# Performance work log

Measured on AMD Instinct MI355X. Metric: run time of the kernel, lower is better.

Reference implementation:

```python
import jax, jax.numpy as jnp
import numpy as np

LAMBDA = 0.7
RATIO = 3
EPS = 1e-6


def setup_inputs() -> dict:
    key = jax.random.key(0)
    k1, k2, k3 = jax.random.split(key, 3)
    bs, n, w, h = 8, 7, 640, 640
    preds = jax.random.normal(k1, (bs, n, w, h), dtype=jnp.float32)
    labels = jax.random.randint(k2, (bs, n, w, h), 0, 2, dtype=jnp.int32)
    training_mask = jax.random.randint(k3, (bs, w, h), 0, 2, dtype=jnp.int32)
    return {"preds": preds, "labels": labels, "training_mask": training_mask}


def _dice(S, G):
    # S, G: [C, P]; per-channel dice coefficient, then mean over channels
    num = 2.0 * jnp.sum(S * G, axis=-1)
    den = jnp.sum(S * S, axis=-1) + jnp.sum(G * G, axis=-1) + EPS
    return jnp.mean(num / den)


def _single_sample(pred, label, mask):
    # pred, label: [n, P]; mask: [P]
    P = pred.shape[-1]
    p = jax.nn.sigmoid(pred)
    pred_n = p[-1] * mask            # masked full-text prediction
    label_n = label[-1] * mask

    # --- OHEM mask M (cal_M): keep all positives + top (ratio*n_pos) hardest negatives ---
    pos = pred_n >= 0.5
    n_pos = jnp.sum(pos)
    n_neg_all = jnp.sum(~pos)
    k = n_pos * RATIO
    # sigmoid outputs are in (0,1); sentinel -1 pushes positives to the end of the descending sort
    neg_vals = jnp.where(pos, -1.0, pred_n)
    sorted_desc = -jnp.sort(-neg_vals)
    thr = sorted_desc[jnp.clip(k - 1, 0, P - 1)]  # k-th largest negative score
    ohem_active = (n_neg_all > k) & (k > 0)
    M = jnp.where(ohem_active, (pred_n >= thr).astype(jnp.float32), 1.0)

    # L_c: dice loss on OHEM-selected full-text map
    L_c = 1.0 - _dice((pred_n * M)[None, :], (label_n * M)[None, :])

    # L_s: dice loss on shrunk kernels, gated by predicted text region W
    W = (pred_n >= 0.5).astype(jnp.float32)
    L_s = 1.0 - _dice(p[:-1] * W, label[:-1] * W)

    loss = LAMBDA * L_c + (1.0 - LAMBDA) * L_s
    return L_c, L_s, loss


def reference(preds, labels, training_mask):
    bs, n, w, h = preds.shape
    preds = preds.reshape(bs, n, w * h)
    labels = labels.reshape(bs, n, w * h).astype(jnp.float32)
    mask = training_mask.reshape(bs, w * h).astype(jnp.float32)
    L_c, L_s, loss = jax.vmap(_single_sample)(preds, labels, mask)
    # reduction='mean'
    return L_c.mean(), L_s.mean(), loss.mean()
```

## Files before the change

### kernel.cpp

```cpp
#include <hip/hip_runtime.h>

#define BS   8
#define NCH  7
#define PX   409600
#define NBIN 65536
#define NCHK 256
#define EPSF 1e-6f
#define NT   256
#define GXA  200
#define UA   2
#define GXB  50
#define UB   4
#define ITB  2
#define NWAVE 1600

__device__ __forceinline__ float sigf(float x) {
    return 1.0f / (1.0f + __expf(-x));
}

__device__ __forceinline__ unsigned wred_u(unsigned v) {
    #pragma unroll
    for (int o = 32; o; o >>= 1) v += __shfl_down(v, o);
    return v;
}

__device__ __forceinline__ float wred_f(float v) {
    #pragma unroll
    for (int o = 32; o; o >>= 1) v += __shfl_down(v, o);
    return v;
}

__device__ __forceinline__ void wred3_f(float& v0, float& v1, float& v2) {
    #pragma unroll
    for (int o = 32; o; o >>= 1) {
        float t0 = __shfl_down(v0, o);
        float t1 = __shfl_down(v1, o);
        float t2 = __shfl_down(v2, o);
        v0 += t0; v1 += t1; v2 += t2;
    }
}

__device__ void select2(const unsigned* __restrict__ chunks,
                        const unsigned* __restrict__ bins,
                        unsigned k, unsigned* out_bin, unsigned* out_rank) {
    __shared__ unsigned cs[256];
    int t = threadIdx.x;
    cs[t] = chunks[t];
    __syncthreads();
    #pragma unroll
    for (int off = 1; off < 256; off <<= 1) {
        unsigned v = cs[t];
        unsigned a = (t + off < 256) ? cs[t + off] : 0u;
        __syncthreads();
        cs[t] = v + a;
        __syncthreads();
    }
    {
        unsigned sfx  = cs[t];
        unsigned sfx1 = (t < 255) ? cs[t + 1] : 0u;
        if (sfx >= k && sfx1 < k) { *out_bin = (unsigned)t; *out_rank = k - sfx1; }
    }
    __syncthreads();
    unsigned chunk = *out_bin, krem = *out_rank;
    cs[t] = bins[chunk * 256 + t];
    __syncthreads();
    #pragma unroll
    for (int off = 1; off < 256; off <<= 1) {
        unsigned v = cs[t];
        unsigned a = (t + off < 256) ? cs[t + off] : 0u;
        __syncthreads();
        cs[t] = v + a;
        __syncthreads();
    }
    {
        unsigned sfx  = cs[t];
        unsigned sfx1 = (t < 255) ? cs[t + 1] : 0u;
        if (sfx >= krem && sfx1 < krem) {
            *out_bin  = chunk * 256 + (unsigned)t;
            *out_rank = krem - sfx1;
        }
    }
    __syncthreads();
}

__global__ __launch_bounds__(256) void k_a(
        const float* __restrict__ preds, const int* __restrict__ labels,
        const int* __restrict__ mask,
        float* __restrict__ psumA,
        unsigned* __restrict__ ppos,
        unsigned* __restrict__ pzero,
        unsigned long long* __restrict__ wm,
        unsigned* __restrict__ done) {
    const int tid = threadIdx.x;
    const int b = blockIdx.y, cb = blockIdx.x;
    if (b == 0 && cb == 0 && tid == 0) *done = 0u;

    const float* pr6 = preds + ((size_t)b * NCH + 6) * PX;
    const int*   lb6 = labels + ((size_t)b * NCH + 6) * PX;
    const int*   mk  = mask + (size_t)b * PX;
    const int g0 = cb * (NT * UA) + tid;
    const int lane = tid & 63, wid = tid >> 6;

    float4 P[UA]; int4 L[UA]; int4 M[UA];
    #pragma unroll
    for (int q = 0; q < UA; q++) {
        int px = (g0 + q * NT) * 4;
        P[q] = *(const float4*)(pr6 + px);
        L[q] = *(const int4*)(lb6 + px);
        M[q] = *(const int4*)(mk + px);
    }

    float a0 = 0.f, a1 = 0.f;
    unsigned a2c = 0, pos = 0, zer = 0;
    #pragma unroll
    for (int q = 0; q < UA; q++) {
        float mm[4]  = {(float)M[q].x, (float)M[q].y, (float)M[q].z, (float)M[q].w};
        float pa[4]  = {P[q].x, P[q].y, P[q].z, P[q].w};
        int   la[4]  = {L[q].x, L[q].y, L[q].z, L[q].w};
        unsigned long long bp[4];
        #pragma unroll
        for (int v = 0; v < 4; v++) {
            float pn = sigf(pa[v]) * mm[v];
            bp[v] = __ballot(pn >= 0.5f);
            unsigned long long bz = __ballot(__float_as_uint(pn) == 0u);
            pos += (unsigned)__popcll(bp[v]);
            zer += (unsigned)__popcll(bz);
            bool ln = (la[v] != 0) & (M[q].x == M[q].x) & (mm[v] != 0.0f);
            a0 += ln ? pn : 0.0f;
            a1 += pn * pn;
            a2c += ln ? 1u : 0u;
        }
        if (lane == 0) {
            int wv = (g0 + q * NT) >> 6;
            ulonglong2* wp = (ulonglong2*)(wm + ((size_t)b * NWAVE + wv) * 4);
            wp[0] = make_ulonglong2(bp[0], bp[1]);
            wp[1] = make_ulonglong2(bp[2], bp[3]);
        }
    }

    __shared__ unsigned cpos[4], czer[4];
    __shared__ float red[4][3];
    if (lane == 0) { cpos[wid] = pos; czer[wid] = zer; }
    float v0 = a0, v1 = a1, v2 = (float)a2c;
    wred3_f(v0, v1, v2);
    if (lane == 0) { red[wid][0] = v0; red[wid][1] = v1; red[wid][2] = v2; }
    __syncthreads();
    if (tid < 3) {
        float tot = red[0][tid] + red[1][tid] + red[2][tid] + red[3][tid];
        psumA[((size_t)b * 3 + tid) * GXA + cb] = tot;
    }
    if (tid == 3) ppos[b * GXA + cb]  = cpos[0] + cpos[1] + cpos[2] + cpos[3];
    if (tid == 4) pzero[b * GXA + cb] = czer[0] + czer[1] + czer[2] + czer[3];
}

__global__ __launch_bounds__(256) void k_b(
        const float* __restrict__ preds, const int* __restrict__ labels,
        const unsigned long long* __restrict__ wm,
        float* __restrict__ psumB) {
    const int tid = threadIdx.x;
    const int y = blockIdx.y;
    const int b = y / 6, c = y % 6;
    const int cb = blockIdx.x;
    const int lane = tid & 63;
    const int widu = __builtin_amdgcn_readfirstlane(tid >> 6);
    const float* pc = preds + ((size_t)b * NCH + c) * PX;
    const int*   lc = labels + ((size_t)b * NCH + c) * PX;
    const unsigned long long* wmb = wm + (size_t)b * NWAVE * 4;

    float sn = 0.f, sp = 0.f;
    unsigned slc = 0;

    for (int it = 0; it < ITB; ++it) {
        const int gbase = cb * (NT * UB * ITB) + it * (NT * UB) + tid;
        float4 P[UB]; int4 L[UB];
        #pragma unroll
        for (int q = 0; q < UB; q++) {
            int px = (gbase + q * NT) * 4;
            P[q] = *(const float4*)(pc + px);
            L[q] = *(const int4*)(lc + px);
        }
        ulonglong2 WA[UB], WB[UB];
        #pragma unroll
        for (int q = 0; q < UB; q++) {
            int wv = ((cb * (NT * UB * ITB) + it * (NT * UB) + q * NT) >> 6) + widu;
            const ulonglong2* wp = (const ulonglong2*)(wmb + (size_t)wv * 4);
            WA[q] = wp[0];
            WB[q] = wp[1];
        }
        #pragma unroll
        for (int q = 0; q < UB; q++) {
            float pa[4] = {P[q].x, P[q].y, P[q].z, P[q].w};
            int   la[4] = {L[q].x, L[q].y, L[q].z, L[q].w};
            unsigned wbit[4] = {
                (unsigned)((WA[q].x >> lane) & 1ull), (unsigned)((WA[q].y >> lane) & 1ull),
                (unsigned)((WB[q].x >> lane) & 1ull), (unsigned)((WB[q].y >> lane) & 1ull) };
            #pragma unroll
            for (int v = 0; v < 4; v++) {
                float s = sigf(pa[v]);
                bool w  = wbit[v] != 0u;
                bool lw = w && (la[v] != 0);
                sn += lw ? s : 0.0f;
                sp += w ? s * s : 0.0f;
                slc += lw ? 1u : 0u;
            }
        }
    }

    __shared__ float red[4][3];
    float v0 = sn, v1 = sp, v2 = (float)slc;
    wred3_f(v0, v1, v2);
    if (lane == 0) { red[tid >> 6][0] = v0; red[tid >> 6][1] = v1; red[tid >> 6][2] = v2; }
    __syncthreads();
    if (tid < 3) {
        float tot = red[0][tid] + red[1][tid] + red[2][tid] + red[3][tid];
        psumB[((size_t)y * 3 + tid) * GXB + cb] = tot;
    }
}

__global__ __launch_bounds__(256) void k_sel(
        const float* __restrict__ preds, const int* __restrict__ labels,
        const int* __restrict__ mask,
        const float* __restrict__ psumA, const float* __restrict__ psumB,
        const unsigned* __restrict__ ppos, const unsigned* __restrict__ pzero,
        unsigned* __restrict__ histws, unsigned* __restrict__ chunkws,
        float* __restrict__ lcls, unsigned* __restrict__ done,
        float* __restrict__ out) {
    const int tid = threadIdx.x;
    const int b = blockIdx.x;
    const int lane = tid & 63, wid = tid >> 6;

    __shared__ float S[21];
    __shared__ unsigned C[2];
    if (tid < 21) S[tid] = 0.f;
    if (tid < 2) C[tid] = 0u;
    __syncthreads();
    {
        unsigned pc = 0, zc = 0;
        for (int i = tid; i < GXA; i += NT) {
            pc += ppos[b * GXA + i];
            zc += pzero[b * GXA + i];
        }
        pc = wred_u(pc); zc = wred_u(zc);
        if (lane == 0) { atomicAdd(&C[0], pc); atomicAdd(&C[1], zc); }
    }
    for (int i = tid; i < 3 * GXA; i += NT)
        atomicAdd(&S[18 + i / GXA], psumA[(size_t)b * 3 * GXA + i]);
    for (int i = tid; i < 6 * 3 * GXB; i += NT) {
        int cch = i / (3 * GXB);
        int j   = (i / GXB) % 3;
        atomicAdd(&S[j * 6 + cch], psumB[(size_t)b * 6 * 3 * GXB + i]);
    }
    __syncthreads();
    const unsigned np = C[0], zc = C[1];

    const unsigned k = np * 3u;
    const bool active = ((unsigned)PX - np > k) && (k > 0u);
    const unsigned nzneg = (unsigned)PX - np - zc;

    float Lc_b;
    if (!active || k >= nzneg) {
        Lc_b = 1.0f - 2.0f * S[18] / (S[19] + S[20] + EPSF);
    } else {
        unsigned* h1 = histws + (size_t)b * NBIN;
        unsigned* c1 = chunkws + (size_t)b * NCHK;
        const float* pr6 = preds + ((size_t)b * NCH + 6) * PX;
        const int*   lb6 = labels + ((size_t)b * NCH + 6) * PX;
        const int*   mk  = mask + (size_t)b * PX;

        for (int j = tid; j < NBIN; j += NT) h1[j] = 0u;
        for (int j = tid; j < NCHK; j += NT) c1[j] = 0u;
        __syncthreads();
        for (int gg = tid; gg < PX; gg += NT) {
            float pnx = sigf(pr6[gg]) * (float)mk[gg];
            if (pnx < 0.5f) {
                unsigned bits = __float_as_uint(pnx);
                if (bits) {
                    atomicAdd(&h1[bits >> 16], 1u);
                    atomicAdd(&c1[bits >> 24], 1u);
                }
            }
        }
        __syncthreads();
        if (tid == 0) { atomicAdd(&h1[0], zc); atomicAdd(&c1[0], zc); }
        __syncthreads();

        __shared__ unsigned rb, rr, rb2, rr2;
        select2(c1, h1, k, &rb, &rr);
        float thrv;
        if (rb == 0u) {
            thrv = 0.0f;
        } else {
            unsigned hi = rb;
            for (int j = tid; j < NBIN; j += NT) h1[j] = 0u;
            for (int j = tid; j < NCHK; j += NT) c1[j] = 0u;
            __syncthreads();
            for (int gg = tid; gg < PX; gg += NT) {
                float pnx = sigf(pr6[gg]) * (float)mk[gg];
                if (pnx < 0.5f) {
                    unsigned bits = __float_as_uint(pnx);
                    if (bits && (bits >> 16) == hi) {
                        unsigned lo = bits & 0xFFFFu;
                        atomicAdd(&h1[lo], 1u);
                        atomicAdd(&c1[lo >> 8], 1u);
                    }
                }
            }
            __syncthreads();
            select2(c1, h1, rr, &rb2, &rr2);
            thrv = __uint_as_float((hi << 16) | rb2);
        }
        float a0 = 0.f, a1 = 0.f, a2 = 0.f;
        for (int gg = tid; gg < PX; gg += NT) {
            float m   = (float)mk[gg];
            float pnx = sigf(pr6[gg]) * m;
            if (pnx >= thrv) {
                float ln = (float)lb6[gg] * m;
                a0 += pnx * ln;
                a1 += pnx * pnx;
                a2 += ln;
            }
        }
        __shared__ float aR[4][3];
        wred3_f(a0, a1, a2);
        if (lane == 0) { aR[wid][0] = a0; aR[wid][1] = a1; aR[wid][2] = a2; }
        __syncthreads();
        float A0 = aR[0][0] + aR[1][0] + aR[2][0] + aR[3][0];
        float A1 = aR[0][1] + aR[1][1] + aR[2][1] + aR[3][1];
        float A2 = aR[0][2] + aR[1][2] + aR[2][2] + aR[3][2];
        Lc_b = 1.0f - 2.0f * A0 / (A1 + A2 + EPSF);
    }

    float ls_acc = 0.f;
    #pragma unroll
    for (int c = 0; c < 6; c++)
        ls_acc += (2.0f * S[c]) / (S[6 + c] + S[12 + c] + EPSF);
    float Ls_b = 1.0f - ls_acc * (1.0f / 6.0f);

    if (tid == 0) {
        lcls[b * 2]     = Lc_b;
        lcls[b * 2 + 1] = Ls_b;
    }

    __shared__ unsigned tick;
    if (tid == 0) {
        __threadfence();
        tick = atomicAdd(done, 1u);
    }
    __syncthreads();
    if (tick != (unsigned)(BS - 1)) return;
    __threadfence();

    float Lc = 0.f, Ls = 0.f;
    if (tid < BS) { Lc = lcls[tid * 2]; Ls = lcls[tid * 2 + 1]; }
    #pragma unroll
    for (int o = 4; o; o >>= 1) { Lc += __shfl_down(Lc, o); Ls += __shfl_down(Ls, o); }
    if (tid == 0) {
        float lc_m = Lc * (1.0f / (float)BS);
        float ls_m = Ls * (1.0f / (float)BS);
        out[0] = lc_m;
        out[1] = ls_m;
        out[2] = 0.7f * lc_m + 0.3f * ls_m;
    }
}

extern "C" void kernel_launch(void* const* d_in, const int* in_sizes, int n_in,
                              void* d_out, int out_size, void* d_ws, size_t ws_size,
                              hipStream_t stream) {
    const float* preds = (const float*)d_in[0];
    const int* labels  = (const int*)d_in[1];
    const int* mask    = (const int*)d_in[2];
    float* out = (float*)d_out;

    unsigned long long* wm = (unsigned long long*)d_ws;
    float*    psumA  = (float*)(wm + (size_t)BS * NWAVE * 4);
    unsigned* ppos   = (unsigned*)(psumA + (size_t)BS * 3 * GXA);
    unsigned* pzero  = ppos + BS * GXA;
    float*    psumB  = (float*)(pzero + BS * GXA);
    unsigned* done   = (unsigned*)(psumB + (size_t)BS * 18 * GXB);
    float*    lcls   = (float*)(done + 8);
    unsigned* histws = (unsigned*)(lcls + BS * 2);
    unsigned* chunkws = histws + (size_t)BS * NBIN;

    hipLaunchKernelGGL(k_a, dim3(GXA, BS), dim3(NT), 0, stream,
                       preds, labels, mask, psumA, ppos, pzero, wm, done);

    hipLaunchKernelGGL(k_b, dim3(GXB, BS * 6), dim3(NT), 0, stream,
                       preds, labels, wm, psumB);

    hipLaunchKernelGGL(k_sel, dim3(BS), dim3(NT), 0, stream,
                       preds, labels, mask, psumA, psumB, ppos, pzero,
                       histws, chunkws, lcls, done, out);
}
```

Measured before the change: 217.3 us.

## Fuse full-text stats and kernel-channel dice passes into one kernel

Merges the two streaming kernels into a single k_main launch. Each channel block recomputes the predicted-text gate W from channel-6 predictions and the mask, instead of reading a ballot bitmask written by an earlier kernel. Channel-0 blocks also accumulate the full-text dice sums, plus positive and zero counts packed into one 16/16-bit counter. This removes one launch and the bitmask round trip through memory. In exchange, channel-6 predictions and the mask are re-read six times per sample, which relies on cache hits, and the sigmoid work is duplicated.

```diff
diff --git a/kernel.cpp b/kernel.cpp
--- a/kernel.cpp
+++ b/kernel.cpp
@@ -7,24 +7,15 @@
 #define NCHK 256
 #define EPSF 1e-6f
 #define NT   256
-#define GXA  200
-#define UA   2
-#define GXB  50
-#define UB   4
-#define ITB  2
-#define NWAVE 1600
+#define GXM  50
+#define UM   4
+#define ITM  2
 
 __device__ __forceinline__ float sigf(float x) {
     return 1.0f / (1.0f + __expf(-x));
 }
 
 __device__ __forceinline__ unsigned wred_u(unsigned v) {
-    #pragma unroll
-    for (int o = 32; o; o >>= 1) v += __shfl_down(v, o);
-    return v;
-}
-
-__device__ __forceinline__ float wred_f(float v) {
     #pragma unroll
     for (int o = 32; o; o >>= 1) v += __shfl_down(v, o);
     return v;
@@ -83,137 +74,111 @@
     __syncthreads();
 }
 
-__global__ __launch_bounds__(256) void k_a(
+__global__ __launch_bounds__(256) void k_main(
         const float* __restrict__ preds, const int* __restrict__ labels,
         const int* __restrict__ mask,
         float* __restrict__ psumA,
         unsigned* __restrict__ ppos,
         unsigned* __restrict__ pzero,
-        unsigned long long* __restrict__ wm,
+        float* __restrict__ psumB,
         unsigned* __restrict__ done) {
-    const int tid = threadIdx.x;
-    const int b = blockIdx.y, cb = blockIdx.x;
-    if (b == 0 && cb == 0 && tid == 0) *done = 0u;
-
-    const float* pr6 = preds + ((size_t)b * NCH + 6) * PX;
-    const int*   lb6 = labels + ((size_t)b * NCH + 6) * PX;
-    const int*   mk  = mask + (size_t)b * PX;
-    const int g0 = cb * (NT * UA) + tid;
-    const int lane = tid & 63, wid = tid >> 6;
-
-    float4 P[UA]; int4 L[UA]; int4 M[UA];
-    #pragma unroll
-    for (int q = 0; q < UA; q++) {
-        int px = (g0 + q * NT) * 4;
-        P[q] = *(const float4*)(pr6 + px);
-        L[q] = *(const int4*)(lb6 + px);
-        M[q] = *(const int4*)(mk + px);
-    }
-
-    float a0 = 0.f, a1 = 0.f;
-    unsigned a2c = 0, pos = 0, zer = 0;
-    #pragma unroll
-    for (int q = 0; q < UA; q++) {
-        float mm[4]  = {(float)M[q].x, (float)M[q].y, (float)M[q].z, (float)M[q].w};
-        float pa[4]  = {P[q].x, P[q].y, P[q].z, P[q].w};
-        int   la[4]  = {L[q].x, L[q].y, L[q].z, L[q].w};
-        unsigned long long bp[4];
-        #pragma unroll
-        for (int v = 0; v < 4; v++) {
-            float pn = sigf(pa[v]) * mm[v];
-            bp[v] = __ballot(pn >= 0.5f);
-            unsigned long long bz = __ballot(__float_as_uint(pn) == 0u);
-            pos += (unsigned)__popcll(bp[v]);
-            zer += (unsigned)__popcll(bz);
-            bool ln = (la[v] != 0) & (M[q].x == M[q].x) & (mm[v] != 0.0f);
-            a0 += ln ? pn : 0.0f;
-            a1 += pn * pn;
-            a2c += ln ? 1u : 0u;
-        }
-        if (lane == 0) {
-            int wv = (g0 + q * NT) >> 6;
-            ulonglong2* wp = (ulonglong2*)(wm + ((size_t)b * NWAVE + wv) * 4);
-            wp[0] = make_ulonglong2(bp[0], bp[1]);
-            wp[1] = make_ulonglong2(bp[2], bp[3]);
-        }
-    }
-
-    __shared__ unsigned cpos[4], czer[4];
-    __shared__ float red[4][3];
-    if (lane == 0) { cpos[wid] = pos; czer[wid] = zer; }
-    float v0 = a0, v1 = a1, v2 = (float)a2c;
-    wred3_f(v0, v1, v2);
-    if (lane == 0) { red[wid][0] = v0; red[wid][1] = v1; red[wid][2] = v2; }
-    __syncthreads();
-    if (tid < 3) {
-        float tot = red[0][tid] + red[1][tid] + red[2][tid] + red[3][tid];
-        psumA[((size_t)b * 3 + tid) * GXA + cb] = tot;
-    }
-    if (tid == 3) ppos[b * GXA + cb]  = cpos[0] + cpos[1] + cpos[2] + cpos[3];
-    if (tid == 4) pzero[b * GXA + cb] = czer[0] + czer[1] + czer[2] + czer[3];
-}
-
-__global__ __launch_bounds__(256) void k_b(
-        const float* __restrict__ preds, const int* __restrict__ labels,
-        const unsigned long long* __restrict__ wm,
-        float* __restrict__ psumB) {
     const int tid = threadIdx.x;
     const int y = blockIdx.y;
     const int b = y / 6, c = y % 6;
     const int cb = blockIdx.x;
-    const int lane = tid & 63;
-    const int widu = __builtin_amdgcn_readfirstlane(tid >> 6);
+    const bool c0 = (c == 0);
+    if (y == 0 && cb == 0 && tid == 0) *done = 0u;
+
     const float* pc = preds + ((size_t)b * NCH + c) * PX;
     const int*   lc = labels + ((size_t)b * NCH + c) * PX;
-    const unsigned long long* wmb = wm + (size_t)b * NWAVE * 4;
+    const float* p6 = preds + ((size_t)b * NCH + 6) * PX;
+    const int*   l6 = labels + ((size_t)b * NCH + 6) * PX;
+    const int*   mk = mask + (size_t)b * PX;
 
     float sn = 0.f, sp = 0.f;
     unsigned slc = 0;
-
-    for (int it = 0; it < ITB; ++it) {
-        const int gbase = cb * (NT * UB * ITB) + it * (NT * UB) + tid;
-        float4 P[UB]; int4 L[UB];
+    float a0 = 0.f, a1 = 0.f;
+    unsigned a2c = 0, cnt = 0;
+
+    for (int it = 0; it < ITM; ++it) {
+        const int gbase = cb * (NT * UM * ITM) + it * (NT * UM) + tid;
+        float4 P6[UM]; int4 M[UM]; float4 P[UM]; int4 L[UM]; int4 L6[UM];
         #pragma unroll
-        for (int q = 0; q < UB; q++) {
+        for (int q = 0; q < UM; q++) {
+            int px = (gbase + q * NT) * 4;
+            P6[q] = *(const float4*)(p6 + px);
+            M[q]  = *(const int4*)(mk + px);
+        }
+        #pragma unroll
+        for (int q = 0; q < UM; q++) {
             int px = (gbase + q * NT) * 4;
             P[q] = *(const float4*)(pc + px);
             L[q] = *(const int4*)(lc + px);
         }
-        ulonglong2 WA[UB], WB[UB];
+        if (c0) {
+            #pragma unroll
+            for (int q = 0; q < UM; q++) {
+                int px = (gbase + q * NT) * 4;
+                L6[q] = *(const int4*)(l6 + px);
+            }
+        }
+        __builtin_amdgcn_sched_barrier(0);
+
         #pragma unroll
-        for (int q = 0; q < UB; q++) {
-            int wv = ((cb * (NT * UB * ITB) + it * (NT * UB) + q * NT) >> 6) + widu;
-            const ulonglong2* wp = (const ulonglong2*)(wmb + (size_t)wv * 4);
-            WA[q] = wp[0];
-            WB[q] = wp[1];
-        }
-        #pragma unroll
-        for (int q = 0; q < UB; q++) {
-            float pa[4] = {P[q].x, P[q].y, P[q].z, P[q].w};
-            int   la[4] = {L[q].x, L[q].y, L[q].z, L[q].w};
-            unsigned wbit[4] = {
-                (unsigned)((WA[q].x >> lane) & 1ull), (unsigned)((WA[q].y >> lane) & 1ull),
-                (unsigned)((WB[q].x >> lane) & 1ull), (unsigned)((WB[q].y >> lane) & 1ull) };
+        for (int q = 0; q < UM; q++) {
+            float mm[4]  = {(float)M[q].x, (float)M[q].y, (float)M[q].z, (float)M[q].w};
+            float p6a[4] = {P6[q].x, P6[q].y, P6[q].z, P6[q].w};
+            float pa[4]  = {P[q].x, P[q].y, P[q].z, P[q].w};
+            int   la[4]  = {L[q].x, L[q].y, L[q].z, L[q].w};
+            int   l6a[4] = {L6[q].x, L6[q].y, L6[q].z, L6[q].w};
             #pragma unroll
             for (int v = 0; v < 4; v++) {
-                float s = sigf(pa[v]);
-                bool w  = wbit[v] != 0u;
-                bool lw = w && (la[v] != 0);
+                float pn = sigf(p6a[v]) * mm[v];
+                bool W   = (pn >= 0.5f);
+                float s  = sigf(pa[v]);
+                bool lw  = W && (la[v] != 0);
                 sn += lw ? s : 0.0f;
-                sp += w ? s * s : 0.0f;
+                sp += W ? s * s : 0.0f;
                 slc += lw ? 1u : 0u;
+                if (c0) {
+                    cnt += W ? 1u : (__float_as_uint(pn) == 0u ? 0x10000u : 0u);
+                    bool ln = (l6a[v] != 0) && (mm[v] != 0.0f);
+                    a0 += ln ? pn : 0.0f;
+                    a1 += pn * pn;
+                    a2c += ln ? 1u : 0u;
+                }
             }
         }
     }
 
     __shared__ float red[4][3];
+    __shared__ float redA[4][3];
+    __shared__ unsigned redC[4];
+    const int lane = tid & 63, wid = tid >> 6;
     float v0 = sn, v1 = sp, v2 = (float)slc;
     wred3_f(v0, v1, v2);
-    if (lane == 0) { red[tid >> 6][0] = v0; red[tid >> 6][1] = v1; red[tid >> 6][2] = v2; }
+    if (lane == 0) { red[wid][0] = v0; red[wid][1] = v1; red[wid][2] = v2; }
+    if (c0) {
+        float u0 = a0, u1 = a1, u2 = (float)a2c;
+        wred3_f(u0, u1, u2);
+        unsigned cr = wred_u(cnt);
+        if (lane == 0) { redA[wid][0] = u0; redA[wid][1] = u1; redA[wid][2] = u2; redC[wid] = cr; }
+    }
     __syncthreads();
     if (tid < 3) {
         float tot = red[0][tid] + red[1][tid] + red[2][tid] + red[3][tid];
-        psumB[((size_t)y * 3 + tid) * GXB + cb] = tot;
+        psumB[((size_t)y * 3 + tid) * GXM + cb] = tot;
+    }
+    if (c0) {
+        if (tid < 3) {
+            float tot = redA[0][tid] + redA[1][tid] + redA[2][tid] + redA[3][tid];
+            psumA[((size_t)b * 3 + tid) * GXM + cb] = tot;
+        }
+        if (tid == 3) {
+            unsigned ct = redC[0] + redC[1] + redC[2] + redC[3];
+            ppos[b * GXM + cb]  = ct & 0xFFFFu;
+            pzero[b * GXM + cb] = ct >> 16;
+        }
     }
 }
 
@@ -236,19 +201,19 @@
     __syncthreads();
     {
         unsigned pc = 0, zc = 0;
-        for (int i = tid; i < GXA; i += NT) {
-            pc += ppos[b * GXA + i];
-            zc += pzero[b * GXA + i];
+        for (int i = tid; i < GXM; i += NT) {
+            pc += ppos[b * GXM + i];
+            zc += pzero[b * GXM + i];
         }
         pc = wred_u(pc); zc = wred_u(zc);
         if (lane == 0) { atomicAdd(&C[0], pc); atomicAdd(&C[1], zc); }
     }
-    for (int i = tid; i < 3 * GXA; i += NT)
-        atomicAdd(&S[18 + i / GXA], psumA[(size_t)b * 3 * GXA + i]);
-    for (int i = tid; i < 6 * 3 * GXB; i += NT) {
-        int cch = i / (3 * GXB);
-        int j   = (i / GXB) % 3;
-        atomicAdd(&S[j * 6 + cch], psumB[(size_t)b * 6 * 3 * GXB + i]);
+    for (int i = tid; i < 3 * GXM; i += NT)
+        atomicAdd(&S[18 + i / GXM], psumA[(size_t)b * 3 * GXM + i]);
+    for (int i = tid; i < 6 * 3 * GXM; i += NT) {
+        int cch = i / (3 * GXM);
+        int j   = (i / GXM) % 3;
+        atomicAdd(&S[j * 6 + cch], psumB[(size_t)b * 6 * 3 * GXM + i]);
     }
     __syncthreads();
     const unsigned np = C[0], zc = C[1];
@@ -371,21 +336,17 @@
     const int* mask    = (const int*)d_in[2];
     float* out = (float*)d_out;
 
-    unsigned long long* wm = (unsigned long long*)d_ws;
-    float*    psumA  = (float*)(wm + (size_t)BS * NWAVE * 4);
-    unsigned* ppos   = (unsigned*)(psumA + (size_t)BS * 3 * GXA);
-    unsigned* pzero  = ppos + BS * GXA;
-    float*    psumB  = (float*)(pzero + BS * GXA);
-    unsigned* done   = (unsigned*)(psumB + (size_t)BS * 18 * GXB);
-    float*    lcls   = (float*)(done + 8);
-    unsigned* histws = (unsigned*)(lcls + BS * 2);
+    float*    psumA   = (float*)d_ws;
+    unsigned* ppos    = (unsigned*)(psumA + (size_t)BS * 3 * GXM);
+    unsigned* pzero   = ppos + BS * GXM;
+    float*    psumB   = (float*)(pzero + BS * GXM);
+    unsigned* done    = (unsigned*)(psumB + (size_t)BS * 18 * GXM);
+    float*    lcls    = (float*)(done + 8);
+    unsigned* histws  = (unsigned*)(lcls + BS * 2);
     unsigned* chunkws = histws + (size_t)BS * NBIN;
 
-    hipLaunchKernelGGL(k_a, dim3(GXA, BS), dim3(NT), 0, stream,
-                       preds, labels, mask, psumA, ppos, pzero, wm, done);
-
-    hipLaunchKernelGGL(k_b, dim3(GXB, BS * 6), dim3(NT), 0, stream,
-                       preds, labels, wm, psumB);
+    hipLaunchKernelGGL(k_main, dim3(GXM, BS * 6), dim3(NT), 0, stream,
+                       preds, labels, mask, psumA, ppos, pzero, psumB, done);
 
     hipLaunchKernelGGL(k_sel, dim3(BS), dim3(NT), 0, stream,
                        preds, labels, mask, psumA, psumB, ppos, pzero,
```

Result: no change. 216.5 us (-0.3%).
